# Optimization experiments

Measured on AMD Instinct MI355X. Metric: run time of the kernel, lower is better.

Reference implementation:

```python
import jax, jax.numpy as jnp
import numpy as np

S, N, A = 64, 4096, 32
HID, DM, NH, DK = 256, 128, 4, 32
EPS = 1e-5
SCALE = float(np.sqrt(DK))


def setup_inputs() -> dict:
    key = jax.random.key(0)
    ks = jax.random.split(key, 20)
    w = lambda i, sh: jax.random.normal(ks[i], sh, jnp.float32) * 0.02
    z = lambda n: jnp.zeros((n,), jnp.float32)
    return {
        "agent_states": jax.random.normal(ks[0], (N, S), jnp.float32),
        "sw1": w(1, (N * S, HID)), "sb1": z(HID),
        "sw2": w(2, (HID, HID)), "sb2": z(HID),
        "sow": w(3, (HID, 64)), "sob": z(64),
        "tw": w(4, (S + 64, DM)), "tb": z(DM),
        "wq": w(5, (DM, DM)), "bq": z(DM),
        "wk": w(6, (DM, DM)), "bk": z(DM),
        "wv": w(7, (DM, DM)), "bv": z(DM),
        "wo": w(8, (DM, DM)), "bo": z(DM),
        "ln_g": jnp.ones((DM,), jnp.float32), "ln_b": z(DM),
        "taw1": w(9, (DM, 64)), "tab1": z(64),
        "taw2": w(10, (64, 32)), "tab2": z(32),
        "ow1": w(11, (S + DM + 32, 256)), "ob1": z(256),
        "ow2": w(12, (256, DM)), "ob2": z(DM),
        "aw": w(13, (DM, A)), "ab": z(A),
        "vw": w(14, (DM, 1)), "vb": z(1),
        "cw": w(15, (S, 64)), "cb": z(64),
        "cdw": w(16, (64, 32)), "cdb": z(32),
    }


def reference(agent_states, sw1, sb1, sw2, sb2, sow, sob, tw, tb,
              wq, bq, wk, bk, wv, bv, wo, bo, ln_g, ln_b,
              taw1, tab1, taw2, tab2, ow1, ob1, ow2, ob2,
              aw, ab, vw, vb, cw, cb, cdw, cdb):
    n = agent_states.shape[0]
    # strategic level: flatten all agent states -> global objective [64]
    gs = agent_states.reshape(-1)
    strat = jax.nn.relu(jax.nn.relu(gs @ sw1 + sb1) @ sw2 + sb2)
    gobj = strat @ sow + sob
    # tactical encode (batched over agents instead of Python loop)
    tact_in = jnp.concatenate(
        [agent_states, jnp.broadcast_to(gobj, (n, gobj.shape[0]))], axis=-1)
    tact = jax.nn.relu(tact_in @ tw + tb)[None]  # [1, n, DM]
    # multi-head attention across agents
    q = (tact @ wq + bq).reshape(1, n, NH, DK).transpose(0, 2, 1, 3)
    k = (tact @ wk + bk).reshape(1, n, NH, DK).transpose(0, 2, 1, 3)
    v = (tact @ wv + bv).reshape(1, n, NH, DK).transpose(0, 2, 1, 3)
    scores = jnp.einsum('bhqd,bhkd->bhqk', q, k) / SCALE
    attn = jax.nn.softmax(scores, axis=-1)  # [1, NH, n, n]
    ctx = jnp.einsum('bhqk,bhkd->bhqd', attn, v).transpose(0, 2, 1, 3).reshape(1, n, DM)
    res = ctx @ wo + bo + tact
    mu = res.mean(-1, keepdims=True)
    var = res.var(-1, keepdims=True)  # biased, like torch LayerNorm
    coord = ((res - mu) / jnp.sqrt(var + EPS) * ln_g + ln_b)[0]  # [n, DM]
    # task allocation (softmax over 32 tasks)
    task = jax.nn.softmax(jax.nn.relu(coord @ taw1 + tab1) @ taw2 + tab2, axis=-1)
    # operational level -> actions / values
    op_in = jnp.concatenate([agent_states, coord, task], axis=-1)
    opf = jax.nn.relu(jax.nn.relu(op_in @ ow1 + ob1) @ ow2 + ob2)
    actions = opf @ aw + ab
    values = opf @ vw + vb
    # communication messages (two stacked linears, no activation in source)
    messages = (agent_states @ cw + cb) @ cdw + cdb
    return actions, values, messages, task, attn, gobj
```

## Files before the change

### kernel.cpp

```cpp
#include <hip/hip_runtime.h>

typedef __attribute__((ext_vector_type(8))) short s8v;
typedef __attribute__((ext_vector_type(4))) short s4v;
typedef __attribute__((ext_vector_type(4))) float f4v;

#define MFMA16(a, b, c) __builtin_amdgcn_mfma_f32_16x16x32_bf16((a), (b), (c), 0, 0, 0)

#define NAG   4096
#define SDIM  64
#define DMOD  128
#define NHD   4
#define DKD   32
#define HIDD  256
static constexpr float INV_SCALE = 0.17677669529663687f;
static constexpr float EPSV = 1e-5f;

#define OFF_ACT   0
#define OFF_VAL   131072
#define OFF_MSG   135168
#define OFF_TASK  266240
#define OFF_ATTN  397312
#define OFF_GOBJ  67506176

static constexpr size_t WS_P1   = 0;
static constexpr size_t WS_P1B  = 524288;
static constexpr size_t WS_P2   = 540672;
static constexpr size_t WS_TACT = 558080;
static constexpr size_t WS_Q    = 2655232;
static constexpr size_t WS_K    = 3703808;
static constexpr size_t WS_VT   = 4752384;
static constexpr size_t WS_CTX  = 5800960;
static constexpr size_t WS_OPIN = 7898112;
static constexpr size_t WS_H    = 9733120;
static constexpr size_t WS_OPF  = 11830272;
static constexpr size_t WS_OW1T = 12878848;
static constexpr size_t WS_OW2T = 12993536;

typedef unsigned short u16;
typedef unsigned int   u32;

static __device__ __forceinline__ u16 f2bf(float f) {
    union { float f; u32 u; } x; x.f = f;
    u32 r = x.u + 0x7FFFu + ((x.u >> 16) & 1u);
    return (u16)(r >> 16);
}
static __device__ __forceinline__ float bf2f(u16 b) {
    union { u32 u; float f; } x; x.u = ((u32)b) << 16;
    return x.f;
}

__global__ __launch_bounds__(256) void k1_sw1(const float* __restrict__ gs,
                                              const float* __restrict__ sw1,
                                              float* __restrict__ p1,
                                              const float* __restrict__ ow1,
                                              const float* __restrict__ ow2,
                                              u16* __restrict__ w1t,
                                              u16* __restrict__ w2t) {
    int tid = threadIdx.x;
    int b = blockIdx.x;
    if (b >= 512) {
        int bb = b - 512;
        if (bb < 224) {
            w1t[tid * 224 + bb] = f2bf(ow1[bb * 256 + tid]);
        } else if (tid < 128) {
            int k0 = (bb - 224) * 8;
#pragma unroll
            for (int kk = 0; kk < 8; ++kk) {
                int k = k0 + kk;
                w2t[tid * 256 + k] = f2bf(ow2[k * 128 + tid]);
            }
        }
        return;
    }
    __shared__ float gsl[512];
    __shared__ float red[4][256];
    gsl[tid]       = gs[b * 512 + tid];
    gsl[tid + 256] = gs[b * 512 + 256 + tid];
    __syncthreads();
    int t = tid & 63;
    int rg = tid >> 6;
    const f4v* w4 = (const f4v*)sw1;
    f4v acc = {0.f, 0.f, 0.f, 0.f};
    size_t rb = (size_t)b * 512;
#pragma unroll 4
    for (int r = rg; r < 512; r += 4) {
        float g = gsl[r];
        f4v w = __builtin_nontemporal_load(&w4[(rb + r) * 64 + t]);
        acc[0] += g * w[0]; acc[1] += g * w[1]; acc[2] += g * w[2]; acc[3] += g * w[3];
    }
    red[rg][4 * t + 0] = acc[0]; red[rg][4 * t + 1] = acc[1];
    red[rg][4 * t + 2] = acc[2]; red[rg][4 * t + 3] = acc[3];
    __syncthreads();
    float s = red[0][tid] + red[1][tid] + red[2][tid] + red[3][tid];
    p1[b * 256 + tid] = s;
}

__global__ void k1b_red(const float* __restrict__ p1, float* __restrict__ p1b) {
    int j = threadIdx.x;
    int b0 = blockIdx.x * 32;
    float s = 0.f;
#pragma unroll
    for (int b = 0; b < 32; ++b) s += p1[(b0 + b) * 256 + j];
    p1b[blockIdx.x * 256 + j] = s;
}

__global__ void k2b_strat(const float* __restrict__ p1b, const float* __restrict__ sb1,
                          const float* __restrict__ sw2, float* __restrict__ p2) {
    __shared__ float h1[256];
    int j = threadIdx.x;
    float s = 0.f;
#pragma unroll
    for (int b = 0; b < 16; ++b) s += p1b[b * 256 + j];
    h1[j] = fmaxf(s + sb1[j], 0.f);
    __syncthreads();
    int i0 = blockIdx.x * 16;
    float acc = 0.f;
#pragma unroll
    for (int i = 0; i < 16; ++i) acc += h1[i0 + i] * sw2[(i0 + i) * 256 + j];
    p2[blockIdx.x * 256 + j] = acc;
}

__global__ __launch_bounds__(256) void k3_tact_qkv(
    const float* __restrict__ p2, const float* __restrict__ sb2,
    const float* __restrict__ sow, const float* __restrict__ sob,
    const float* __restrict__ as, const float* __restrict__ tw, const float* __restrict__ tb,
    const float* __restrict__ wq, const float* __restrict__ bq,
    const float* __restrict__ wk, const float* __restrict__ bk,
    const float* __restrict__ wv, const float* __restrict__ bv,
    float* __restrict__ out_gobj, float* __restrict__ tactws,
    u16* __restrict__ qws, u16* __restrict__ kws, u16* __restrict__ vtws) {
    __shared__ float strat[256];
    __shared__ float gobj[64];
    __shared__ float asl[8][64];
    __shared__ float tl[8][128];
    int tid = threadIdx.x;
    int a0 = blockIdx.x * 8;
    {
        float s = 0.f;
#pragma unroll
        for (int b = 0; b < 16; ++b) s += p2[b * 256 + tid];
        strat[tid] = fmaxf(s + sb2[tid], 0.f);
    }
#pragma unroll
    for (int r = 0; r < 2; ++r) {
        int idx = tid + r * 256;
        asl[idx >> 6][idx & 63] = as[a0 * 64 + idx];
    }
    __syncthreads();
    if (tid < 64) {
        float g = sob[tid];
        for (int i = 0; i < 256; ++i) g += strat[i] * sow[i * 64 + tid];
        gobj[tid] = g;
        if (blockIdx.x == 0) out_gobj[tid] = g;
    }
    __syncthreads();
    int ah = tid >> 7, j = tid & 127;
    float gacc = 0.f;
    for (int i = 0; i < 64; ++i) gacc += gobj[i] * tw[(64 + i) * 128 + j];
    float acc[4];
    float base = tb[j] + gacc;
#pragma unroll
    for (int a = 0; a < 4; ++a) acc[a] = base;
    for (int i = 0; i < 64; ++i) {
        float w = tw[i * 128 + j];
#pragma unroll
        for (int a = 0; a < 4; ++a) acc[a] += asl[ah * 4 + a][i] * w;
    }
#pragma unroll
    for (int a = 0; a < 4; ++a) {
        float t = fmaxf(acc[a], 0.f);
        tl[ah * 4 + a][j] = t;
        tactws[(size_t)(a0 + ah * 4 + a) * 128 + j] = t;
    }
    __syncthreads();
    int h = j >> 5, d = j & 31;
#pragma unroll
    for (int a = 0; a < 4; ++a) acc[a] = 0.f;
    for (int i = 0; i < 128; ++i) {
        float w = wq[i * 128 + j];
#pragma unroll
        for (int a = 0; a < 4; ++a) acc[a] += tl[ah * 4 + a][i] * w;
    }
#pragma unroll
    for (int a = 0; a < 4; ++a)
        qws[h * 131072 + (a0 + ah * 4 + a) * 32 + d] = f2bf((acc[a] + bq[j]) * INV_SCALE);
#pragma unroll
    for (int a = 0; a < 4; ++a) acc[a] = 0.f;
    for (int i = 0; i < 128; ++i) {
        float w = wk[i * 128 + j];
#pragma unroll
        for (int a = 0; a < 4; ++a) acc[a] += tl[ah * 4 + a][i] * w;
    }
#pragma unroll
    for (int a = 0; a < 4; ++a)
        kws[h * 131072 + (a0 + ah * 4 + a) * 32 + d] = f2bf(acc[a] + bk[j]);
#pragma unroll
    for (int a = 0; a < 4; ++a) acc[a] = 0.f;
    for (int i = 0; i < 128; ++i) {
        float w = wv[i * 128 + j];
#pragma unroll
        for (int a = 0; a < 4; ++a) acc[a] += tl[ah * 4 + a][i] * w;
    }
    union { u16 u[4]; s4v v; } pk;
#pragma unroll
    for (int a = 0; a < 4; ++a) pk.u[a] = f2bf(acc[a] + bv[j]);
    *(s4v*)(vtws + h * 131072 + d * 4096 + a0 + ah * 4) = pk.v;
}

__global__ __launch_bounds__(512) void k4_attn(
    const u16* __restrict__ qws, const u16* __restrict__ kws, const u16* __restrict__ vtws,
    float* __restrict__ attn, float* __restrict__ ctxws) {
    int tid = threadIdx.x;
    int wid = tid >> 6;
    int l = tid & 63;
    int g = l >> 4;
    int ln = l & 15;
    int h = blockIdx.x >> 8;
    int qt = (blockIdx.x & 255) * 16;
    const u16* qh = qws + h * 131072;
    const u16* kh = kws + h * 131072;
    const u16* vh = vtws + h * 131072;
    int j0 = wid * 512;

    s8v aq = *(const s8v*)(qh + (qt + ln) * 32 + 8 * g);
    f4v zero = {0.f, 0.f, 0.f, 0.f};

    __shared__ __align__(16) union SmemU {
        struct {
            float red[8][16];
            u16 ldsPb[8][2][16][40];
            float pctx[8][16][32];
        } a;
        float sT[2][16][260];
    } sm;

    f4v lacc = zero, accA = zero, accB = zero;
    int buf = 0;
    for (int jc = 0; jc < 16; ++jc) {
        int jb = j0 + jc * 32;
        s8v b0 = *(const s8v*)(kh + (jb + ln) * 32 + 8 * g);
        s8v b1 = *(const s8v*)(kh + (jb + 16 + ln) * 32 + 8 * g);
        f4v S0 = MFMA16(aq, b0, zero);
        f4v S1 = MFMA16(aq, b1, zero);
#pragma unroll
        for (int r = 0; r < 4; ++r) {
            float w0 = __expf(S0[r]);
            float w1 = __expf(S1[r]);
            lacc[r] += w0 + w1;
            sm.a.ldsPb[wid][buf][4 * g + r][ln] = f2bf(w0);
            sm.a.ldsPb[wid][buf][4 * g + r][16 + ln] = f2bf(w1);
        }
        s8v bp = *(const s8v*)&sm.a.ldsPb[wid][buf][ln][8 * g];
        s8v va = *(const s8v*)(vh + ln * 4096 + jb + 8 * g);
        s8v vb = *(const s8v*)(vh + (16 + ln) * 4096 + jb + 8 * g);
        accA = MFMA16(va, bp, accA);
        accB = MFMA16(vb, bp, accB);
        buf ^= 1;
    }
#pragma unroll
    for (int m = 1; m <= 8; m <<= 1) {
        lacc[0] += __shfl_xor(lacc[0], m);
        lacc[1] += __shfl_xor(lacc[1], m);
        lacc[2] += __shfl_xor(lacc[2], m);
        lacc[3] += __shfl_xor(lacc[3], m);
    }
    if (ln == 0) {
#pragma unroll
        for (int r = 0; r < 4; ++r) sm.a.red[wid][4 * g + r] = lacc[r];
    }
    __syncthreads();
    float linvq = 1.f / (sm.a.red[0][ln] + sm.a.red[1][ln] + sm.a.red[2][ln] + sm.a.red[3][ln] +
                         sm.a.red[4][ln] + sm.a.red[5][ln] + sm.a.red[6][ln] + sm.a.red[7][ln]);
#pragma unroll
    for (int r = 0; r < 4; ++r) {
        sm.a.pctx[wid][ln][4 * g + r] = accA[r] * linvq;
        sm.a.pctx[wid][ln][16 + 4 * g + r] = accB[r] * linvq;
    }
    __syncthreads();
    {
        int q = tid >> 5;
        int d = tid & 31;
        float s = sm.a.pctx[0][q][d] + sm.a.pctx[1][q][d] + sm.a.pctx[2][q][d] + sm.a.pctx[3][q][d] +
                  sm.a.pctx[4][q][d] + sm.a.pctx[5][q][d] + sm.a.pctx[6][q][d] + sm.a.pctx[7][q][d];
        ctxws[(size_t)(qt + q) * 128 + h * 32 + d] = s;
    }
    __syncthreads();

    float* attnh = attn + (size_t)h * 4096 * 4096;
    auto COMPUTE = [&](int c, int p) {
        int co = wid * 32;
        int jb = c * 256 + co;
        s8v b0 = *(const s8v*)(kh + (jb + ln) * 32 + 8 * g);
        s8v b1 = *(const s8v*)(kh + (jb + 16 + ln) * 32 + 8 * g);
        f4v S0 = MFMA16(b0, aq, zero);
        f4v S1 = MFMA16(b1, aq, zero);
        f4v o0, o1;
#pragma unroll
        for (int r = 0; r < 4; ++r) {
            o0[r] = __expf(S0[r]) * linvq;
            o1[r] = __expf(S1[r]) * linvq;
        }
        *(f4v*)&sm.sT[p][ln][co + 4 * g] = o0;
        *(f4v*)&sm.sT[p][ln][co + 16 + 4 * g] = o1;
    };
    auto STORE = [&](int c, int p) {
#pragma unroll
        for (int r2 = 0; r2 < 2; ++r2) {
            int row = 2 * wid + r2;
            f4v t = *(const f4v*)&sm.sT[p][row][4 * l];
            *(f4v*)(attnh + (size_t)(qt + row) * 4096 + c * 256 + 4 * l) = t;
        }
    };
    COMPUTE(0, 0);
    __syncthreads();
    for (int c = 1; c < 16; ++c) {
        STORE(c - 1, (c - 1) & 1);
        COMPUTE(c, c & 1);
        __syncthreads();
    }
    STORE(15, 1);
}

__global__ __launch_bounds__(512) void k5_post(
    const float* __restrict__ ctxws, const float* __restrict__ tactws,
    const float* __restrict__ wo, const float* __restrict__ bo,
    const float* __restrict__ lng, const float* __restrict__ lnb,
    const float* __restrict__ taw1, const float* __restrict__ tab1,
    const float* __restrict__ taw2, const float* __restrict__ tab2,
    const float* __restrict__ as, float* __restrict__ dout, u16* __restrict__ opin) {
    __shared__ float wos[128 * 128];
    __shared__ float tw1s[128 * 64];
    __shared__ float tw2s[64 * 32];
    __shared__ float cx[8][128];
    __shared__ float coords[8][128];
    __shared__ float t1v[8][64];
    int tid = threadIdx.x;
    for (int i = tid; i < 128 * 128; i += 512) wos[i] = wo[i];
    for (int i = tid; i < 128 * 64; i += 512) tw1s[i] = taw1[i];
    for (int i = tid; i < 64 * 32; i += 512) tw2s[i] = taw2[i];
    __syncthreads();
    int w = tid >> 6, l = tid & 63;
    for (int it = 0; it < 2; ++it) {
        int n = blockIdx.x * 16 + w * 2 + it;
        float c0 = ctxws[(size_t)n * 128 + l], c1 = ctxws[(size_t)n * 128 + 64 + l];
        float t0 = tactws[(size_t)n * 128 + l], t1 = tactws[(size_t)n * 128 + 64 + l];
        float av = as[n * 64 + l];
        cx[w][l] = c0; cx[w][64 + l] = c1;
        float r0 = bo[l] + t0, r1 = bo[64 + l] + t1;
        for (int k = 0; k < 128; ++k) {
            float cv = cx[w][k];
            r0 += cv * wos[k * 128 + l];
            r1 += cv * wos[k * 128 + 64 + l];
        }
        float s = r0 + r1;
#pragma unroll
        for (int m = 1; m <= 32; m <<= 1) s += __shfl_xor(s, m);
        float mu = s * (1.f / 128.f);
        float d0 = r0 - mu, d1 = r1 - mu;
        float vs = d0 * d0 + d1 * d1;
#pragma unroll
        for (int m = 1; m <= 32; m <<= 1) vs += __shfl_xor(vs, m);
        float rstd = 1.f / sqrtf(vs * (1.f / 128.f) + EPSV);
        float co0 = d0 * rstd * lng[l] + lnb[l];
        float co1 = d1 * rstd * lng[64 + l] + lnb[64 + l];
        coords[w][l] = co0; coords[w][64 + l] = co1;
        opin[(size_t)n * 224 + l] = f2bf(av);
        opin[(size_t)n * 224 + 64 + l] = f2bf(co0);
        opin[(size_t)n * 224 + 128 + l] = f2bf(co1);
        float a1 = tab1[l];
        for (int i = 0; i < 128; ++i) a1 += coords[w][i] * tw1s[i * 64 + l];
        t1v[w][l] = fmaxf(a1, 0.f);
        if (l < 32) {
            float a2 = tab2[l];
            for (int i = 0; i < 64; ++i) a2 += t1v[w][i] * tw2s[i * 32 + l];
            float mx = a2;
#pragma unroll
            for (int m = 1; m <= 16; m <<= 1) mx = fmaxf(mx, __shfl_xor(mx, m));
            float e = __expf(a2 - mx);
            float se = e;
#pragma unroll
            for (int m = 1; m <= 16; m <<= 1) se += __shfl_xor(se, m);
            float tk = e / se;
            dout[OFF_TASK + n * 32 + l] = tk;
            opin[(size_t)n * 224 + 192 + l] = f2bf(tk);
        }
    }
}

__global__ __launch_bounds__(256) void k6a(const u16* __restrict__ opin, const u16* __restrict__ w1t,
                                           const float* __restrict__ ob1, u16* __restrict__ Hws) {
    int tid = threadIdx.x;
    int w = tid >> 6, l = tid & 63, g = l >> 4, ln = l & 15;
    int bm = blockIdx.x & 63, bn = blockIdx.x >> 6;
    int m0 = bm * 64 + w * 16, n0 = bn * 64;
    f4v acc[4];
    f4v zero = {0.f, 0.f, 0.f, 0.f};
#pragma unroll
    for (int nt = 0; nt < 4; ++nt) acc[nt] = zero;
    for (int kt = 0; kt < 7; ++kt) {
        s8v A = *(const s8v*)(opin + (size_t)(m0 + ln) * 224 + kt * 32 + 8 * g);
#pragma unroll
        for (int nt = 0; nt < 4; ++nt) {
            s8v B = *(const s8v*)(w1t + (size_t)(n0 + nt * 16 + ln) * 224 + kt * 32 + 8 * g);
            acc[nt] = MFMA16(A, B, acc[nt]);
        }
    }
#pragma unroll
    for (int nt = 0; nt < 4; ++nt) {
        int col = n0 + nt * 16 + ln;
        float bias = ob1[col];
#pragma unroll
        for (int r = 0; r < 4; ++r) {
            int row = m0 + 4 * g + r;
            Hws[(size_t)row * 256 + col] = f2bf(fmaxf(acc[nt][r] + bias, 0.f));
        }
    }
}

__global__ __launch_bounds__(256) void k6b(const u16* __restrict__ Hws, const u16* __restrict__ w2t,
                                           const float* __restrict__ ob2, u16* __restrict__ opfws) {
    int tid = threadIdx.x;
    int w = tid >> 6, l = tid & 63, g = l >> 4, ln = l & 15;
    int bm = blockIdx.x & 63, bn = blockIdx.x >> 6;
    int m0 = bm * 64 + w * 16, n0 = bn * 64;
    f4v acc[4];
    f4v zero = {0.f, 0.f, 0.f, 0.f};
#pragma unroll
    for (int nt = 0; nt < 4; ++nt) acc[nt] = zero;
    for (int kt = 0; kt < 8; ++kt) {
        s8v A = *(const s8v*)(Hws + (size_t)(m0 + ln) * 256 + kt * 32 + 8 * g);
#pragma unroll
        for (int nt = 0; nt < 4; ++nt) {
            s8v B = *(const s8v*)(w2t + (size_t)(n0 + nt * 16 + ln) * 256 + kt * 32 + 8 * g);
            acc[nt] = MFMA16(A, B, acc[nt]);
        }
    }
#pragma unroll
    for (int nt = 0; nt < 4; ++nt) {
        int col = n0 + nt * 16 + ln;
        float bias = ob2[col];
#pragma unroll
        for (int r = 0; r < 4; ++r) {
            int row = m0 + 4 * g + r;
            opfws[(size_t)row * 128 + col] = f2bf(fmaxf(acc[nt][r] + bias, 0.f));
        }
    }
}

__global__ __launch_bounds__(256) void k6c(const u16* __restrict__ opf, const float* __restrict__ as,
                                           const float* __restrict__ aw, const float* __restrict__ ab,
                                           const float* __restrict__ vw, const float* __restrict__ vb,
                                           const float* __restrict__ cw, const float* __restrict__ cb,
                                           const float* __restrict__ cdw, const float* __restrict__ cdb,
                                           float* __restrict__ dout) {
    __shared__ float opfs[4][128];
    __shared__ float asl[4][64];
    __shared__ float m1s[4][64];
    int tid = threadIdx.x;
    int w = tid >> 6, l = tid & 63;
    int n = blockIdx.x * 4 + w;
    {
        u32 u = *(const u32*)(opf + (size_t)n * 128 + 2 * l);
        opfs[w][2 * l] = bf2f((u16)(u & 0xffff));
        opfs[w][2 * l + 1] = bf2f((u16)(u >> 16));
        asl[w][l] = as[n * 64 + l];
    }
    __syncthreads();
    if (l < 32) {
        float a = ab[l];
        for (int k = 0; k < 128; ++k) a += opfs[w][k] * aw[k * 32 + l];
        dout[OFF_ACT + n * 32 + l] = a;
    }
    {
        float p = opfs[w][l] * vw[l] + opfs[w][64 + l] * vw[64 + l];
#pragma unroll
        for (int m = 1; m <= 32; m <<= 1) p += __shfl_xor(p, m);
        if (l == 0) dout[OFF_VAL + n] = p + vb[0];
    }
    {
        float a = cb[l];
        for (int k = 0; k < 64; ++k) a += asl[w][k] * cw[k * 64 + l];
        m1s[w][l] = a;
    }
    __syncthreads();
    if (l < 32) {
        float a = cdb[l];
        for (int k = 0; k < 64; ++k) a += m1s[w][k] * cdw[k * 32 + l];
        dout[OFF_MSG + n * 32 + l] = a;
    }
}

extern "C" void kernel_launch(void* const* d_in, const int* in_sizes, int n_in,
                              void* d_out, int out_size, void* d_ws, size_t ws_size,
                              hipStream_t stream) {
    const float* as  = (const float*)d_in[0];
    const float* sw1 = (const float*)d_in[1];
    const float* sb1 = (const float*)d_in[2];
    const float* sw2 = (const float*)d_in[3];
    const float* sb2 = (const float*)d_in[4];
    const float* sow = (const float*)d_in[5];
    const float* sob = (const float*)d_in[6];
    const float* tw  = (const float*)d_in[7];
    const float* tb  = (const float*)d_in[8];
    const float* wq  = (const float*)d_in[9];
    const float* bq  = (const float*)d_in[10];
    const float* wk  = (const float*)d_in[11];
    const float* bk  = (const float*)d_in[12];
    const float* wv  = (const float*)d_in[13];
    const float* bv  = (const float*)d_in[14];
    const float* wo  = (const float*)d_in[15];
    const float* bo  = (const float*)d_in[16];
    const float* lng = (const float*)d_in[17];
    const float* lnb = (const float*)d_in[18];
    const float* taw1 = (const float*)d_in[19];
    const float* tab1 = (const float*)d_in[20];
    const float* taw2 = (const float*)d_in[21];
    const float* tab2 = (const float*)d_in[22];
    const float* ow1 = (const float*)d_in[23];
    const float* ob1 = (const float*)d_in[24];
    const float* ow2 = (const float*)d_in[25];
    const float* ob2 = (const float*)d_in[26];
    const float* aw  = (const float*)d_in[27];
    const float* ab  = (const float*)d_in[28];
    const float* vw  = (const float*)d_in[29];
    const float* vb  = (const float*)d_in[30];
    const float* cw  = (const float*)d_in[31];
    const float* cb  = (const float*)d_in[32];
    const float* cdw = (const float*)d_in[33];
    const float* cdb = (const float*)d_in[34];

    float* dout = (float*)d_out;
    char* ws = (char*)d_ws;
    float* p1    = (float*)(ws + WS_P1);
    float* p1b   = (float*)(ws + WS_P1B);
    float* p2    = (float*)(ws + WS_P2);
    float* tactw = (float*)(ws + WS_TACT);
    u16*   qws   = (u16*)(ws + WS_Q);
    u16*   kws   = (u16*)(ws + WS_K);
    u16*   vtws  = (u16*)(ws + WS_VT);
    float* ctxws = (float*)(ws + WS_CTX);
    u16*   opin  = (u16*)(ws + WS_OPIN);
    u16*   Hws   = (u16*)(ws + WS_H);
    u16*   opfws = (u16*)(ws + WS_OPF);
    u16*   w1t   = (u16*)(ws + WS_OW1T);
    u16*   w2t   = (u16*)(ws + WS_OW2T);

    hipLaunchKernelGGL(k1_sw1, dim3(768), dim3(256), 0, stream, as, sw1, p1, ow1, ow2, w1t, w2t);
    hipLaunchKernelGGL(k1b_red, dim3(16), dim3(256), 0, stream, p1, p1b);
    hipLaunchKernelGGL(k2b_strat, dim3(16), dim3(256), 0, stream, p1b, sb1, sw2, p2);
    hipLaunchKernelGGL(k3_tact_qkv, dim3(512), dim3(256), 0, stream,
                       p2, sb2, sow, sob, as, tw, tb, wq, bq, wk, bk, wv, bv,
                       dout + OFF_GOBJ, tactw, qws, kws, vtws);
    hipLaunchKernelGGL(k4_attn, dim3(1024), dim3(512), 0, stream,
                       qws, kws, vtws, dout + OFF_ATTN, ctxws);
    hipLaunchKernelGGL(k5_post, dim3(256), dim3(512), 0, stream,
                       ctxws, tactw, wo, bo, lng, lnb, taw1, tab1, taw2, tab2, as, dout, opin);
    hipLaunchKernelGGL(k6a, dim3(256), dim3(256), 0, stream, opin, w1t, ob1, Hws);
    hipLaunchKernelGGL(k6b, dim3(128), dim3(256), 0, stream, Hws, w2t, ob2, opfws);
    hipLaunchKernelGGL(k6c, dim3(1024), dim3(256), 0, stream,
                       opfws, as, aw, ab, vw, vb, cw, cb, cdw, cdb, dout);
}
```

Before: 193.4 us.

## Fuse P·V accumulation into normalized attention write pass

The first pass over keys now only accumulates softmax row sums; the P·V MFMA work moves into the second pass. There it reuses the already-normalized probabilities staged in shared memory for the attention store, converting them to bf16 as MFMA operands. This removes the duplicated LDS staging of unnormalized probabilities and shrinks the shared-memory union. In exchange, the second pass carries the V loads and MFMAs, and the context uses bf16 of normalized probabilities, so rounding differs slightly.

```diff
diff --git a/kernel.cpp b/kernel.cpp
--- a/kernel.cpp
+++ b/kernel.cpp
@@ -226,16 +226,12 @@
     f4v zero = {0.f, 0.f, 0.f, 0.f};
 
     __shared__ __align__(16) union SmemU {
-        struct {
-            float red[8][16];
-            u16 ldsPb[8][2][16][40];
-            float pctx[8][16][32];
-        } a;
+        float red[8][16];
         float sT[2][16][260];
+        float pctx[8][16][32];
     } sm;
 
-    f4v lacc = zero, accA = zero, accB = zero;
-    int buf = 0;
+    f4v lacc = zero;
     for (int jc = 0; jc < 16; ++jc) {
         int jb = j0 + jc * 32;
         s8v b0 = *(const s8v*)(kh + (jb + ln) * 32 + 8 * g);
@@ -243,19 +239,8 @@
         f4v S0 = MFMA16(aq, b0, zero);
         f4v S1 = MFMA16(aq, b1, zero);
 #pragma unroll
-        for (int r = 0; r < 4; ++r) {
-            float w0 = __expf(S0[r]);
-            float w1 = __expf(S1[r]);
-            lacc[r] += w0 + w1;
-            sm.a.ldsPb[wid][buf][4 * g + r][ln] = f2bf(w0);
-            sm.a.ldsPb[wid][buf][4 * g + r][16 + ln] = f2bf(w1);
-        }
-        s8v bp = *(const s8v*)&sm.a.ldsPb[wid][buf][ln][8 * g];
-        s8v va = *(const s8v*)(vh + ln * 4096 + jb + 8 * g);
-        s8v vb = *(const s8v*)(vh + (16 + ln) * 4096 + jb + 8 * g);
-        accA = MFMA16(va, bp, accA);
-        accB = MFMA16(vb, bp, accB);
-        buf ^= 1;
+        for (int r = 0; r < 4; ++r)
+            lacc[r] += __expf(S0[r]) + __expf(S1[r]);
     }
 #pragma unroll
     for (int m = 1; m <= 8; m <<= 1) {
@@ -266,29 +251,17 @@
     }
     if (ln == 0) {
 #pragma unroll
-        for (int r = 0; r < 4; ++r) sm.a.red[wid][4 * g + r] = lacc[r];
-    }
-    __syncthreads();
-    float linvq = 1.f / (sm.a.red[0][ln] + sm.a.red[1][ln] + sm.a.red[2][ln] + sm.a.red[3][ln] +
-                         sm.a.red[4][ln] + sm.a.red[5][ln] + sm.a.red[6][ln] + sm.a.red[7][ln]);
-#pragma unroll
-    for (int r = 0; r < 4; ++r) {
-        sm.a.pctx[wid][ln][4 * g + r] = accA[r] * linvq;
-        sm.a.pctx[wid][ln][16 + 4 * g + r] = accB[r] * linvq;
-    }
-    __syncthreads();
-    {
-        int q = tid >> 5;
-        int d = tid & 31;
-        float s = sm.a.pctx[0][q][d] + sm.a.pctx[1][q][d] + sm.a.pctx[2][q][d] + sm.a.pctx[3][q][d] +
-                  sm.a.pctx[4][q][d] + sm.a.pctx[5][q][d] + sm.a.pctx[6][q][d] + sm.a.pctx[7][q][d];
-        ctxws[(size_t)(qt + q) * 128 + h * 32 + d] = s;
-    }
+        for (int r = 0; r < 4; ++r) sm.red[wid][4 * g + r] = lacc[r];
+    }
+    __syncthreads();
+    float linvq = 1.f / (sm.red[0][ln] + sm.red[1][ln] + sm.red[2][ln] + sm.red[3][ln] +
+                         sm.red[4][ln] + sm.red[5][ln] + sm.red[6][ln] + sm.red[7][ln]);
     __syncthreads();
 
     float* attnh = attn + (size_t)h * 4096 * 4096;
+    f4v accA = zero, accB = zero;
+    int co = wid * 32;
     auto COMPUTE = [&](int c, int p) {
-        int co = wid * 32;
         int jb = c * 256 + co;
         s8v b0 = *(const s8v*)(kh + (jb + ln) * 32 + 8 * g);
         s8v b1 = *(const s8v*)(kh + (jb + 16 + ln) * 32 + 8 * g);
@@ -303,7 +276,17 @@
         *(f4v*)&sm.sT[p][ln][co + 4 * g] = o0;
         *(f4v*)&sm.sT[p][ln][co + 16 + 4 * g] = o1;
     };
-    auto STORE = [&](int c, int p) {
+    auto PVSTORE = [&](int c, int p) {
+        int jb = c * 256 + co;
+        f4v t0 = *(const f4v*)&sm.sT[p][ln][co + 8 * g];
+        f4v t1 = *(const f4v*)&sm.sT[p][ln][co + 8 * g + 4];
+        union { u16 u[8]; s8v v; } bp;
+#pragma unroll
+        for (int i = 0; i < 4; ++i) { bp.u[i] = f2bf(t0[i]); bp.u[4 + i] = f2bf(t1[i]); }
+        s8v va = *(const s8v*)(vh + ln * 4096 + jb + 8 * g);
+        s8v vb = *(const s8v*)(vh + (16 + ln) * 4096 + jb + 8 * g);
+        accA = MFMA16(va, bp.v, accA);
+        accB = MFMA16(vb, bp.v, accB);
 #pragma unroll
         for (int r2 = 0; r2 < 2; ++r2) {
             int row = 2 * wid + r2;
@@ -314,11 +297,26 @@
     COMPUTE(0, 0);
     __syncthreads();
     for (int c = 1; c < 16; ++c) {
-        STORE(c - 1, (c - 1) & 1);
+        PVSTORE(c - 1, (c - 1) & 1);
         COMPUTE(c, c & 1);
         __syncthreads();
     }
-    STORE(15, 1);
+    PVSTORE(15, 1);
+    __syncthreads();
+
+#pragma unroll
+    for (int r = 0; r < 4; ++r) {
+        sm.pctx[wid][ln][4 * g + r] = accA[r];
+        sm.pctx[wid][ln][16 + 4 * g + r] = accB[r];
+    }
+    __syncthreads();
+    {
+        int q = tid >> 5;
+        int d = tid & 31;
+        float s = sm.pctx[0][q][d] + sm.pctx[1][q][d] + sm.pctx[2][q][d] + sm.pctx[3][q][d] +
+                  sm.pctx[4][q][d] + sm.pctx[5][q][d] + sm.pctx[6][q][d] + sm.pctx[7][q][d];
+        ctxws[(size_t)(qt + q) * 128 + h * 32 + d] = s;
+    }
 }
 
 __global__ __launch_bounds__(512) void k5_post(
```

Result: no change. 190.2 us, median of 2 (-1.6%).
